# Kernel optimization log

Hardware: AMD Instinct MI355X
Metric: run time of the kernel (lower is better)

Reference implementation:

```python
import jax, jax.numpy as jnp
import numpy as np

# Config from module init / global Args
H = 8        # n_head
DK = 64      # d_k
DV = 64      # d_v
D = 512      # d_model
KSZ = 3      # kernel_size (args.kernel_size)
B_PARAM = 0.001
CUR_HEAD = 3
ALPHA_C = -float(np.log(B_PARAM / (H - 1) * CUR_HEAD))  # alpha_c (nonzero head)
EPS = 1e-6


def setup_inputs() -> dict:
    key = jax.random.key(0)
    ks = jax.random.split(key, 8)
    B, L = 2, 2048
    q = jax.random.normal(ks[0], (B, L, D), jnp.float32)
    k = jax.random.normal(ks[1], (B, L, D), jnp.float32)
    v = jax.random.normal(ks[2], (B, L, D), jnp.float32)
    # Linear weights stored torch-style: [out_features, in_features]
    w_q = jax.random.normal(ks[3], (H * DK, D), jnp.float32) * 0.02
    w_k = jax.random.normal(ks[4], (H * DK, D), jnp.float32) * 0.02
    w_v = jax.random.normal(ks[5], (H * DV, D), jnp.float32) * 0.02
    w_fc = jax.random.normal(ks[6], (D, H * DV), jnp.float32) * 0.02
    gamma = jnp.ones((D,), jnp.float32)
    beta = jnp.zeros((D,), jnp.float32)
    return {"q": q, "k": k, "v": v, "w_q": w_q, "w_k": w_k, "w_v": w_v,
            "w_fc": w_fc, "gamma": gamma, "beta": beta}


def reference(q, k, v, w_q, w_k, w_v, w_fc, gamma, beta):
    B, L, _ = q.shape
    residual = q
    # QKV projections -> [B, H, L, d]
    qh = jnp.einsum('bld,ed->ble', q, w_q).reshape(B, L, H, DK).transpose(0, 2, 1, 3)
    kh = jnp.einsum('bld,ed->ble', k, w_k).reshape(B, L, H, DK).transpose(0, 2, 1, 3)
    vh = jnp.einsum('bld,ed->ble', v, w_v).reshape(B, L, H, DV).transpose(0, 2, 1, 3)
    # Scores: matmul(q / sqrt(d_k), k^T)  (LaSAttention receives d_k = d_k**0.5)
    attn = jnp.einsum('bhqd,bhkd->bhqk', qh, kh) / jnp.sqrt(jnp.float32(DK))
    # Distance weighting: eld = alpha_c * -(x - y) * attn, d_l[i,j] = j - i
    idx = jnp.arange(L)
    d_l = idx[None, :] - idx[:, None]                      # [L, L]
    eld_mat = (-ALPHA_C * d_l).astype(attn.dtype)
    eld = eld_mat[None, None, :, :] * attn
    # Softmax then avg_pool1d(kernel=KSZ, stride=1, pad=(KSZ-1)//2, count_include_pad)
    p = jax.nn.softmax(eld, axis=-1)                       # [B, H, L, L]
    pad = (KSZ - 1) // 2
    pp = jnp.pad(p, ((0, 0), (0, 0), (0, 0), (pad, pad)))
    pooled = sum(pp[..., j:j + L] for j in range(KSZ)) / jnp.float32(KSZ)
    # Value matmul (seq lengths equal so no trimming needed)
    out = jnp.einsum('bhqk,bhkd->bhqd', pooled, vh)
    out = out.transpose(0, 2, 1, 3).reshape(B, L, H * DV)
    # Output projection (dropout is identity in eval), residual, LayerNorm
    out = jnp.einsum('ble,de->bld', out, w_fc)
    out = out[:, :, None, :] + residual[:, :, None, :]     # [B, L, 1, D]
    mu = out.mean(axis=-1, keepdims=True)
    var = ((out - mu) ** 2).mean(axis=-1, keepdims=True)
    out = (out - mu) / jnp.sqrt(var + EPS) * gamma + beta
    return (out, pooled)
```

## Files before the change

### kernel.cpp

```cpp
#include <hip/hip_runtime.h>
#include <cstddef>
#include <cstdint>

#define ALPHA_C 7.7550531393693407f
constexpr int BB = 2;
constexpr int LL = 2048;
constexpr int HH = 8;
constexpr size_t OUT0  = (size_t)BB * LL * 512;
constexpr size_t PLANE = (size_t)BB * HH * LL * 64;
constexpr size_t XN    = (size_t)BB * LL * 512;
constexpr size_t WN    = (size_t)512 * 512;

typedef __attribute__((ext_vector_type(8))) short bf16x8;
typedef __attribute__((ext_vector_type(4))) short short4v;
typedef __attribute__((ext_vector_type(4))) float f32x4;

__device__ inline short f2bf(float x) {
  union { float f; unsigned u; } un; un.f = x;
  unsigned r = un.u + 0x7fffu + ((un.u >> 16) & 1u);
  return (short)(r >> 16);
}
__device__ inline float bf2f(short s) {
  union { unsigned u; float f; } un; un.u = ((unsigned)(unsigned short)s) << 16;
  return un.f;
}
__device__ inline void split3(float x, short& h, short& m, short& l) {
  h = f2bf(x); float r = x - bf2f(h);
  m = f2bf(r); float r2 = r - bf2f(m);
  l = f2bf(r2);
}

__global__ __launch_bounds__(256) void k_split3x(
    const float* __restrict__ a, const float* __restrict__ b, const float* __restrict__ c,
    short* __restrict__ da, short* __restrict__ db, short* __restrict__ dc, size_t n)
{
  size_t i = ((size_t)blockIdx.x * 256 + threadIdx.x) * 4;
  if (i >= n) return;
  const float* srcs[3] = {a, b, c};
  short* dsts[3] = {da, db, dc};
  #pragma unroll
  for (int s = 0; s < 3; ++s) {
    float4 x = *(const float4*)&srcs[s][i];
    short4v h, m, l;
    short th, tm, tl;
    split3(x.x, th, tm, tl); h[0] = th; m[0] = tm; l[0] = tl;
    split3(x.y, th, tm, tl); h[1] = th; m[1] = tm; l[1] = tl;
    split3(x.z, th, tm, tl); h[2] = th; m[2] = tm; l[2] = tl;
    split3(x.w, th, tm, tl); h[3] = th; m[3] = tm; l[3] = tl;
    *(short4v*)&dsts[s][i]         = h;
    *(short4v*)&dsts[s][n + i]     = m;
    *(short4v*)&dsts[s][2 * n + i] = l;
  }
}

__global__ __launch_bounds__(256) void k_cvtbf(
    const float* __restrict__ src, short* __restrict__ dst, size_t n)
{
  size_t i = ((size_t)blockIdx.x * 256 + threadIdx.x) * 8;
  if (i >= n) return;
  float4 a = *(const float4*)&src[i];
  float4 b = *(const float4*)&src[i + 4];
  bf16x8 o;
  o[0] = f2bf(a.x); o[1] = f2bf(a.y); o[2] = f2bf(a.z); o[3] = f2bf(a.w);
  o[4] = f2bf(b.x); o[5] = f2bf(b.y); o[6] = f2bf(b.z); o[7] = f2bf(b.w);
  *(bf16x8*)&dst[i] = o;
}

__global__ __launch_bounds__(256) void k_vavg(
    const short* __restrict__ vt, short* __restrict__ vavgt)
{
  const size_t row = blockIdx.x;
  const short* src = vt + row * LL;
  short* dst = vavgt + row * LL;
  const int c0 = threadIdx.x * 8;
  bf16x8 x = *(const bf16x8*)&src[c0];
  float xf[10];
  xf[0] = (c0 > 0) ? bf2f(src[c0 - 1]) : 0.f;
  #pragma unroll
  for (int i = 0; i < 8; ++i) xf[i + 1] = bf2f(x[i]);
  xf[9] = (c0 + 8 < LL) ? bf2f(src[c0 + 8]) : 0.f;
  bf16x8 o;
  #pragma unroll
  for (int i = 0; i < 8; ++i) o[i] = f2bf((xf[i] + xf[i + 1] + xf[i + 2]) * (1.0f / 3.0f));
  *(bf16x8*)&dst[c0] = o;
}

__global__ __launch_bounds__(256) void k_proj(
    const short* __restrict__ xq, const short* __restrict__ xk, const short* __restrict__ xv,
    const short* __restrict__ wq3, const short* __restrict__ wk3, const short* __restrict__ wv3,
    short* __restrict__ qs, short* __restrict__ ks, short* __restrict__ vt)
{
  const int bx  = blockIdx.x;
  const int sel = bx >> 3;
  const int n0  = (bx & 7) * 64;
  const int m0  = blockIdx.y * 64;
  const short* X = sel == 0 ? xq  : (sel == 1 ? xk  : xv);
  const short* W = sel == 0 ? wq3 : (sel == 1 ? wk3 : wv3);

  __shared__ short Xs[3][64 * 72];
  __shared__ short Ws[3][64 * 72];
  const int tid = threadIdx.x;
  const int lane = tid & 63, w = tid >> 6;
  const int quad = lane >> 4, l15 = lane & 15, colg = l15;
  const int sr8 = tid >> 3, sc8 = (tid & 7) * 8;

  f32x4 acc[4];
  #pragma unroll
  for (int t = 0; t < 4; ++t) { acc[t][0]=0.f; acc[t][1]=0.f; acc[t][2]=0.f; acc[t][3]=0.f; }

  for (int kt = 0; kt < 8; ++kt) {
    const int k0 = kt * 64;
    #pragma unroll
    for (int p = 0; p < 3; ++p) {
      #pragma unroll
      for (int it = 0; it < 2; ++it) {
        int r = it * 32 + sr8;
        *(bf16x8*)&Xs[p][r * 72 + sc8] = *(const bf16x8*)&X[p * XN + (size_t)(m0 + r) * 512 + k0 + sc8];
        *(bf16x8*)&Ws[p][r * 72 + sc8] = *(const bf16x8*)&W[p * WN + (size_t)(n0 + r) * 512 + k0 + sc8];
      }
    }
    __syncthreads();
    #pragma unroll
    for (int ch = 0; ch < 2; ++ch) {
      const int ka = (quad << 3) + ch * 32;
      const int ar = (w * 16 + l15) * 72 + ka;
      bf16x8 ah = *(const bf16x8*)&Xs[0][ar];
      bf16x8 am = *(const bf16x8*)&Xs[1][ar];
      bf16x8 al = *(const bf16x8*)&Xs[2][ar];
      #pragma unroll
      for (int t = 0; t < 4; ++t) {
        const int br = (t * 16 + l15) * 72 + ka;
        bf16x8 bh_ = *(const bf16x8*)&Ws[0][br];
        bf16x8 bm_ = *(const bf16x8*)&Ws[1][br];
        bf16x8 bl_ = *(const bf16x8*)&Ws[2][br];
        acc[t] = __builtin_amdgcn_mfma_f32_16x16x32_bf16(ah, bh_, acc[t], 0, 0, 0);
        acc[t] = __builtin_amdgcn_mfma_f32_16x16x32_bf16(ah, bm_, acc[t], 0, 0, 0);
        acc[t] = __builtin_amdgcn_mfma_f32_16x16x32_bf16(am, bh_, acc[t], 0, 0, 0);
        acc[t] = __builtin_amdgcn_mfma_f32_16x16x32_bf16(ah, bl_, acc[t], 0, 0, 0);
        acc[t] = __builtin_amdgcn_mfma_f32_16x16x32_bf16(al, bh_, acc[t], 0, 0, 0);
        acc[t] = __builtin_amdgcn_mfma_f32_16x16x32_bf16(am, bm_, acc[t], 0, 0, 0);
      }
    }
    __syncthreads();
  }

  if (sel < 2) {
    short* Y = sel == 0 ? qs : ks;
    #pragma unroll
    for (int t = 0; t < 4; ++t) {
      const int e = n0 + t * 16 + colg, h = e >> 6, dk = e & 63;
      #pragma unroll
      for (int r = 0; r < 4; ++r) {
        const int m = m0 + w * 16 + quad * 4 + r;
        const int b = m >> 11, l = m & 2047;
        size_t base = ((size_t)(b * HH + h) * LL + l) * 64 + dk;
        short hh, mm, ll; split3(acc[t][r], hh, mm, ll);
        Y[base] = hh; Y[PLANE + base] = mm; Y[2 * PLANE + base] = ll;
      }
    }
  } else {
    const int b  = m0 >> 11;
    const int l0 = (m0 & 2047) + w * 16 + quad * 4;
    #pragma unroll
    for (int t = 0; t < 4; ++t) {
      const int e = n0 + t * 16 + colg, h = e >> 6, dk = e & 63;
      short4v s;
      #pragma unroll
      for (int r = 0; r < 4; ++r) s[r] = f2bf(acc[t][r]);
      *(short4v*)&vt[(((size_t)b * HH + h) * 64 + dk) * LL + l0] = s;
    }
  }
}

__global__ __launch_bounds__(256) void k_stats(
    const short* __restrict__ qs, const short* __restrict__ ks,
    float* __restrict__ statspart)
{
  const int i0 = blockIdx.x * 64;
  const int jh = blockIdx.y;
  const int bh = blockIdx.z;
  __shared__ short Ks[3][64 * 72];
  const int tid = threadIdx.x;
  const int lane = tid & 63, w = tid >> 6;
  const int quad = lane >> 4, colg = lane & 15, l15 = lane & 15;
  const int sr8 = tid >> 3, sc8 = (tid & 7) * 8;

  bf16x8 qf[3][2];
  {
    const size_t qoff = ((size_t)bh * LL + i0 + w * 16 + l15) * 64 + (quad << 3);
    #pragma unroll
    for (int p = 0; p < 3; ++p)
      #pragma unroll
      for (int ch = 0; ch < 2; ++ch)
        qf[p][ch] = *(const bf16x8*)&qs[p * PLANE + qoff + ch * 32];
  }

  const int jt0 = jh * 16;
  const short* kbase = ks + (size_t)bh * LL * 64;
  #pragma unroll
  for (int p = 0; p < 3; ++p)
    #pragma unroll
    for (int it = 0; it < 2; ++it) {
      int r = it * 32 + sr8;
      *(bf16x8*)&Ks[p][r * 72 + sc8] =
          *(const bf16x8*)&kbase[p * PLANE + ((size_t)jt0 * 64 + r) * 64 + sc8];
    }
  __syncthreads();

  float M[4], S[4];
  #pragma unroll
  for (int r = 0; r < 4; ++r) { M[r] = -3.0e38f; S[r] = 0.f; }

  for (int jj = 0; jj < 16; ++jj) {
    const int jt = jt0 + jj;
    const int j0 = jt * 64;
    bf16x8 kreg[3][2];
    if (jj + 1 < 16) {
      #pragma unroll
      for (int p = 0; p < 3; ++p)
        #pragma unroll
        for (int it = 0; it < 2; ++it) {
          int r = it * 32 + sr8;
          kreg[p][it] = *(const bf16x8*)&kbase[p * PLANE + ((size_t)(jt + 1) * 64 + r) * 64 + sc8];
        }
    }

    f32x4 acc[4];
    #pragma unroll
    for (int t = 0; t < 4; ++t) { acc[t][0]=0.f; acc[t][1]=0.f; acc[t][2]=0.f; acc[t][3]=0.f; }
    #pragma unroll
    for (int ch = 0; ch < 2; ++ch) {
      const int ka = (quad << 3) + ch * 32;
      #pragma unroll
      for (int t = 0; t < 4; ++t) {
        const int br = (t * 16 + l15) * 72 + ka;
        bf16x8 bh_ = *(const bf16x8*)&Ks[0][br];
        bf16x8 bm_ = *(const bf16x8*)&Ks[1][br];
        bf16x8 bl_ = *(const bf16x8*)&Ks[2][br];
        acc[t] = __builtin_amdgcn_mfma_f32_16x16x32_bf16(qf[0][ch], bh_, acc[t], 0, 0, 0);
        acc[t] = __builtin_amdgcn_mfma_f32_16x16x32_bf16(qf[0][ch], bm_, acc[t], 0, 0, 0);
        acc[t] = __builtin_amdgcn_mfma_f32_16x16x32_bf16(qf[1][ch], bh_, acc[t], 0, 0, 0);
        acc[t] = __builtin_amdgcn_mfma_f32_16x16x32_bf16(qf[0][ch], bl_, acc[t], 0, 0, 0);
        acc[t] = __builtin_amdgcn_mfma_f32_16x16x32_bf16(qf[2][ch], bh_, acc[t], 0, 0, 0);
        acc[t] = __builtin_amdgcn_mfma_f32_16x16x32_bf16(qf[1][ch], bm_, acc[t], 0, 0, 0);
      }
    }

    #pragma unroll
    for (int r = 0; r < 4; ++r) {
      const int irow = i0 + w * 16 + quad * 4 + r;
      float e0 = -ALPHA_C * (float)(j0 +  0 + colg - irow) * (acc[0][r] * 0.125f);
      float e1 = -ALPHA_C * (float)(j0 + 16 + colg - irow) * (acc[1][r] * 0.125f);
      float e2 = -ALPHA_C * (float)(j0 + 32 + colg - irow) * (acc[2][r] * 0.125f);
      float e3 = -ALPHA_C * (float)(j0 + 48 + colg - irow) * (acc[3][r] * 0.125f);
      float mx = fmaxf(fmaxf(e0, e1), fmaxf(e2, e3));
      float nM = fmaxf(M[r], mx);
      S[r] = S[r] * __expf(M[r] - nM)
           + __expf(e0 - nM) + __expf(e1 - nM) + __expf(e2 - nM) + __expf(e3 - nM);
      M[r] = nM;
    }

    __syncthreads();
    if (jj + 1 < 16) {
      #pragma unroll
      for (int p = 0; p < 3; ++p)
        #pragma unroll
        for (int it = 0; it < 2; ++it) {
          int r = it * 32 + sr8;
          *(bf16x8*)&Ks[p][r * 72 + sc8] = kreg[p][it];
        }
    }
    __syncthreads();
  }

  #pragma unroll
  for (int r = 0; r < 4; ++r) {
    float M_ = M[r], S_ = S[r];
    #pragma unroll
    for (int d = 1; d < 16; d <<= 1) {
      float Mo = __shfl_xor(M_, d);
      float So = __shfl_xor(S_, d);
      float nM = fmaxf(M_, Mo);
      S_ = S_ * __expf(M_ - nM) + So * __expf(Mo - nM);
      M_ = nM;
    }
    if (colg == 0) {
      int irow = i0 + w * 16 + quad * 4 + r;
      size_t idx = (((size_t)jh * 16 + bh) * LL + irow) * 2;
      statspart[idx] = M_; statspart[idx + 1] = S_;
    }
  }
}

__global__ __launch_bounds__(256) void k_mergestats(
    const float* __restrict__ statspart, float* __restrict__ rowstats)
{
  const size_t row = (size_t)blockIdx.x * 256 + threadIdx.x;
  float2 a = *(const float2*)&statspart[row * 2];
  float2 b = *(const float2*)&statspart[(size_t)16 * LL * 2 + row * 2];
  float nM = fmaxf(a.x, b.x);
  float S = a.y * __expf(a.x - nM) + b.y * __expf(b.x - nM);
  rowstats[row * 2] = nM; rowstats[row * 2 + 1] = S;
}

__global__ __launch_bounds__(256) void k_pool_pv(
    const short* __restrict__ qs, const short* __restrict__ ks,
    const short* __restrict__ vavgt, const float* __restrict__ rowstats,
    float* __restrict__ pooled, short* __restrict__ outh)
{
  const int i0 = blockIdx.x * 64;
  const int bh = blockIdx.y;
  const int b = bh >> 3, h = bh & 7;
  float*       Pg = pooled + (size_t)bh * LL * LL;
  const short* Vt = vavgt + (size_t)bh * 64 * LL;
  const short* kbase = ks + (size_t)bh * LL * 64;

  __shared__ short Ks[3][64 * 72];
  __shared__ short Vsm[64 * 72];
  __shared__ short Pa[2][64 * 72];
  __shared__ float Mrow[64], invSr[64], lhalo[64];

  const int tid = threadIdx.x;
  const int lane = tid & 63, w = tid >> 6;
  const int quad = lane >> 4, colg = lane & 15, l15 = lane & 15;
  const int sr8 = tid >> 3, sc8 = (tid & 7) * 8;

  bf16x8 qf[3][2];
  {
    const size_t qoff = ((size_t)bh * LL + i0 + w * 16 + l15) * 64 + (quad << 3);
    #pragma unroll
    for (int p = 0; p < 3; ++p)
      #pragma unroll
      for (int ch = 0; ch < 2; ++ch)
        qf[p][ch] = *(const bf16x8*)&qs[p * PLANE + qoff + ch * 32];
  }
  if (tid < 64) {
    float2 ms = *(const float2*)&rowstats[((size_t)bh * LL + i0 + tid) * 2];
    Mrow[tid] = ms.x; invSr[tid] = 1.0f / ms.y; lhalo[tid] = 0.f;
  }

  #pragma unroll
  for (int p = 0; p < 3; ++p)
    #pragma unroll
    for (int it = 0; it < 2; ++it) {
      int r = it * 32 + sr8;
      *(bf16x8*)&Ks[p][r * 72 + sc8] = *(const bf16x8*)&kbase[p * PLANE + (size_t)r * 64 + sc8];
    }
  __syncthreads();

  f32x4 pv[4];
  #pragma unroll
  for (int t = 0; t < 4; ++t) { pv[t][0]=0.f; pv[t][1]=0.f; pv[t][2]=0.f; pv[t][3]=0.f; }

  for (int jt = 0; jt <= 32; ++jt) {
    if (jt < 32) {
      const int j0 = jt * 64;
      f32x4 acc[4];
      #pragma unroll
      for (int t = 0; t < 4; ++t) { acc[t][0]=0.f; acc[t][1]=0.f; acc[t][2]=0.f; acc[t][3]=0.f; }
      #pragma unroll
      for (int ch = 0; ch < 2; ++ch) {
        const int ka = (quad << 3) + ch * 32;
        #pragma unroll
        for (int t = 0; t < 4; ++t) {
          const int br = (t * 16 + l15) * 72 + ka;
          bf16x8 bh_ = *(const bf16x8*)&Ks[0][br];
          bf16x8 bm_ = *(const bf16x8*)&Ks[1][br];
          bf16x8 bl_ = *(const bf16x8*)&Ks[2][br];
          acc[t] = __builtin_amdgcn_mfma_f32_16x16x32_bf16(qf[0][ch], bh_, acc[t], 0, 0, 0);
          acc[t] = __builtin_amdgcn_mfma_f32_16x16x32_bf16(qf[0][ch], bm_, acc[t], 0, 0, 0);
          acc[t] = __builtin_amdgcn_mfma_f32_16x16x32_bf16(qf[1][ch], bh_, acc[t], 0, 0, 0);
          acc[t] = __builtin_amdgcn_mfma_f32_16x16x32_bf16(qf[0][ch], bl_, acc[t], 0, 0, 0);
          acc[t] = __builtin_amdgcn_mfma_f32_16x16x32_bf16(qf[2][ch], bh_, acc[t], 0, 0, 0);
          acc[t] = __builtin_amdgcn_mfma_f32_16x16x32_bf16(qf[1][ch], bm_, acc[t], 0, 0, 0);
        }
      }
      short* Pc = Pa[jt & 1];
      #pragma unroll
      for (int r = 0; r < 4; ++r) {
        const int row = w * 16 + quad * 4 + r;
        const int irow = i0 + row;
        const float Mr = Mrow[row], iS = invSr[row];
        #pragma unroll
        for (int t = 0; t < 4; ++t) {
          int jl = t * 16 + colg;
          float e = -ALPHA_C * (float)(j0 + jl - irow) * (acc[t][r] * 0.125f);
          Pc[row * 72 + jl] = f2bf(__expf(e - Mr) * iS);
        }
      }
    }
    if (jt >= 1) {
      #pragma unroll
      for (int it = 0; it < 2; ++it) {
        int d = it * 32 + sr8;
        *(bf16x8*)&Vsm[d * 72 + sc8] = *(const bf16x8*)&Vt[(size_t)d * LL + (jt - 1) * 64 + sc8];
      }
    }
    __syncthreads();

    if (jt >= 1) {
      const short* Pp = Pa[(jt - 1) & 1];
      const short* Pn = Pa[jt & 1];
      #pragma unroll
      for (int u = 0; u < 2; ++u) {
        const int row = (u == 0) ? (tid >> 3) : (tid >> 3) + 32;
        const int c0 = (tid & 7) * 8;
        bf16x8 x = *(const bf16x8*)&Pp[row * 72 + c0];
        float xf[8];
        #pragma unroll
        for (int i = 0; i < 8; ++i) xf[i] = bf2f(x[i]);
        float lft = (c0 == 0)  ? lhalo[row] : bf2f(Pp[row * 72 + c0 - 1]);
        float rgt = (c0 == 56) ? ((jt < 32) ? bf2f(Pn[row * 72]) : 0.f)
                               : bf2f(Pp[row * 72 + c0 + 8]);
        f32x4 o0, o1;
        o0[0] = (lft   + xf[0] + xf[1]) * (1.0f/3.0f);
        o0[1] = (xf[0] + xf[1] + xf[2]) * (1.0f/3.0f);
        o0[2] = (xf[1] + xf[2] + xf[3]) * (1.0f/3.0f);
        o0[3] = (xf[2] + xf[3] + xf[4]) * (1.0f/3.0f);
        o1[0] = (xf[3] + xf[4] + xf[5]) * (1.0f/3.0f);
        o1[1] = (xf[4] + xf[5] + xf[6]) * (1.0f/3.0f);
        o1[2] = (xf[5] + xf[6] + xf[7]) * (1.0f/3.0f);
        o1[3] = (xf[6] + xf[7] + rgt  ) * (1.0f/3.0f);
        float* dst = &Pg[(size_t)(i0 + row) * LL + (jt - 1) * 64 + c0];
        __builtin_nontemporal_store(o0, (f32x4*)dst);
        __builtin_nontemporal_store(o1, (f32x4*)(dst + 4));
        if (c0 == 56) lhalo[row] = xf[7];
      }
      #pragma unroll
      for (int ch = 0; ch < 2; ++ch) {
        const int ka = (quad << 3) + ch * 32;
        bf16x8 af = *(const bf16x8*)&Pp[(w * 16 + l15) * 72 + ka];
        #pragma unroll
        for (int t = 0; t < 4; ++t) {
          bf16x8 bfv = *(const bf16x8*)&Vsm[(t * 16 + l15) * 72 + ka];
          pv[t] = __builtin_amdgcn_mfma_f32_16x16x32_bf16(af, bfv, pv[t], 0, 0, 0);
        }
      }
    }
    if (jt + 1 < 32) {
      #pragma unroll
      for (int p = 0; p < 3; ++p)
        #pragma unroll
        for (int it = 0; it < 2; ++it) {
          int r = it * 32 + sr8;
          *(bf16x8*)&Ks[p][r * 72 + sc8] =
              *(const bf16x8*)&kbase[p * PLANE + ((size_t)(jt + 1) * 64 + r) * 64 + sc8];
        }
    }
    __syncthreads();
  }

  #pragma unroll
  for (int t = 0; t < 4; ++t)
    #pragma unroll
    for (int r = 0; r < 4; ++r) {
      int i = i0 + w * 16 + quad * 4 + r;
      int d = t * 16 + colg;
      outh[((size_t)b * LL + i) * 512 + h * 64 + d] = f2bf(pv[t][r]);
    }
}

__global__ __launch_bounds__(256) void k_fc(
    const short* __restrict__ outh, const short* __restrict__ wfcb, float* __restrict__ fcout)
{
  const int n0 = blockIdx.x * 64;
  const int m0 = blockIdx.y * 64;
  __shared__ short Asm[64 * 72];
  __shared__ short Bsm[64 * 72];
  const int tid = threadIdx.x;
  const int lane = tid & 63, w = tid >> 6;
  const int sr8 = tid >> 3, sc8 = (tid & 7) * 8;

  f32x4 acc[4];
  #pragma unroll
  for (int t = 0; t < 4; ++t) { acc[t][0]=0.f; acc[t][1]=0.f; acc[t][2]=0.f; acc[t][3]=0.f; }

  for (int k0 = 0; k0 < 512; k0 += 64) {
    #pragma unroll
    for (int it = 0; it < 2; ++it) {
      int r = it * 32 + sr8;
      *(bf16x8*)&Asm[r * 72 + sc8] = *(const bf16x8*)&outh[(size_t)(m0 + r) * 512 + k0 + sc8];
      *(bf16x8*)&Bsm[r * 72 + sc8] = *(const bf16x8*)&wfcb[(size_t)(n0 + r) * 512 + k0 + sc8];
    }
    __syncthreads();
    #pragma unroll
    for (int ch = 0; ch < 2; ++ch) {
      const int ka = ((lane >> 4) << 3) + ch * 32;
      bf16x8 af = *(const bf16x8*)&Asm[(w * 16 + (lane & 15)) * 72 + ka];
      #pragma unroll
      for (int t = 0; t < 4; ++t) {
        bf16x8 bfv = *(const bf16x8*)&Bsm[(t * 16 + (lane & 15)) * 72 + ka];
        acc[t] = __builtin_amdgcn_mfma_f32_16x16x32_bf16(af, bfv, acc[t], 0, 0, 0);
      }
    }
    __syncthreads();
  }
  const int q4 = lane >> 4, colg = lane & 15;
  #pragma unroll
  for (int t = 0; t < 4; ++t)
    #pragma unroll
    for (int r = 0; r < 4; ++r) {
      int m = m0 + w * 16 + q4 * 4 + r;
      fcout[(size_t)m * 512 + n0 + t * 16 + colg] = acc[t][r];
    }
}

__global__ __launch_bounds__(256) void k_ln(
    const float* __restrict__ fcout, const float* __restrict__ resid,
    const float* __restrict__ gamma, const float* __restrict__ beta,
    float* __restrict__ out)
{
  const size_t row = blockIdx.x;
  const int tid = threadIdx.x;
  __shared__ float red[256];

  float x0 = fcout[row * 512 + tid]       + resid[row * 512 + tid];
  float x1 = fcout[row * 512 + 256 + tid] + resid[row * 512 + 256 + tid];

  red[tid] = x0 + x1; __syncthreads();
  for (int off = 128; off > 0; off >>= 1) {
    if (tid < off) red[tid] += red[tid + off];
    __syncthreads();
  }
  const float mu = red[0] * (1.0f / 512.0f); __syncthreads();

  float d0 = x0 - mu, d1 = x1 - mu;
  red[tid] = d0 * d0 + d1 * d1; __syncthreads();
  for (int off = 128; off > 0; off >>= 1) {
    if (tid < off) red[tid] += red[tid + off];
    __syncthreads();
  }
  const float var = red[0] * (1.0f / 512.0f);
  const float rstd = 1.0f / sqrtf(var + 1e-6f);

  out[row * 512 + tid]       = d0 * rstd * gamma[tid]       + beta[tid];
  out[row * 512 + 256 + tid] = d1 * rstd * gamma[tid + 256] + beta[tid + 256];
}

extern "C" void kernel_launch(void* const* d_in, const int* in_sizes, int n_in,
                              void* d_out, int out_size, void* d_ws, size_t ws_size,
                              hipStream_t stream)
{
  const float* q     = (const float*)d_in[0];
  const float* k     = (const float*)d_in[1];
  const float* v     = (const float*)d_in[2];
  const float* wq    = (const float*)d_in[3];
  const float* wk    = (const float*)d_in[4];
  const float* wv    = (const float*)d_in[5];
  const float* wfc   = (const float*)d_in[6];
  const float* gamma = (const float*)d_in[7];
  const float* beta  = (const float*)d_in[8];

  float* out    = (float*)d_out;
  float* pooled = out + OUT0;

  short* xq    = (short*)d_ws;
  short* xk    = xq + 3 * XN;
  short* xv    = xk + 3 * XN;
  short* wq3   = xv + 3 * XN;
  short* wk3   = wq3 + 3 * WN;
  short* wv3   = wk3 + 3 * WN;
  short* qsp   = wv3 + 3 * WN;
  short* ksp   = qsp + 3 * PLANE;
  short* vt    = ksp + 3 * PLANE;
  short* vavgt = vt + PLANE;
  short* wfcb  = vavgt + PLANE;
  short* outh  = wfcb + WN;
  float* statspart = (float*)(outh + OUT0);
  float* rowstats  = statspart + 4 * (size_t)BB * HH * LL;
  float* fcout     = rowstats + 2 * (size_t)BB * HH * LL;

  k_split3x<<<dim3((unsigned)(XN / 4 / 256)), 256, 0, stream>>>(q, k, v, xq, xk, xv, XN);
  k_split3x<<<dim3((unsigned)(WN / 4 / 256)), 256, 0, stream>>>(wq, wk, wv, wq3, wk3, wv3, WN);
  k_cvtbf  <<<dim3((unsigned)(WN / 8 / 256)), 256, 0, stream>>>(wfc, wfcb, WN);
  k_proj   <<<dim3(24, 64), 256, 0, stream>>>(xq, xk, xv, wq3, wk3, wv3, qsp, ksp, vt);
  k_vavg   <<<dim3(1024),   256, 0, stream>>>(vt, vavgt);
  k_stats  <<<dim3(32, 2, 16), 256, 0, stream>>>(qsp, ksp, statspart);
  k_mergestats<<<dim3(128), 256, 0, stream>>>(statspart, rowstats);
  k_pool_pv<<<dim3(32, 16), 256, 0, stream>>>(qsp, ksp, vavgt, rowstats, pooled, outh);
  k_fc     <<<dim3(8, 64),  256, 0, stream>>>(outh, wfcb, fcout);
  k_ln     <<<dim3(4096),   256, 0, stream>>>(fcout, q, gamma, beta, out);
}
```

Baseline: 496.7 us.

## Cache unnormalized exp scores in bf16 to skip recomputing QK in pool pass

The stats kernel now writes per-tile unnormalized exponentials (bf16) and per-tile running maxima to a large workspace buffer. The pool/PV kernel reads these back and rescales them instead of recomputing the 6-pass split-bf16 QK^T MFMA product. It is also split into two j-halves with a partial-sum merge kernel for more parallelism. This trades heavy MFMA recompute for an extra 128MB write and read of bf16 scores, plus an extra launch, and reuses the input-split workspace region for the score buffer.

```diff
diff --git a/kernel.cpp b/kernel.cpp
--- a/kernel.cpp
+++ b/kernel.cpp
@@ -10,6 +10,7 @@
 constexpr size_t PLANE = (size_t)BB * HH * LL * 64;
 constexpr size_t XN    = (size_t)BB * LL * 512;
 constexpr size_t WN    = (size_t)512 * 512;
+constexpr size_t UGN   = (size_t)BB * HH * LL * LL;
 
 typedef __attribute__((ext_vector_type(8))) short bf16x8;
 typedef __attribute__((ext_vector_type(4))) short short4v;
@@ -172,14 +173,16 @@
   }
 }
 
-__global__ __launch_bounds__(256) void k_stats(
+__global__ __launch_bounds__(256) void k_stats_u(
     const short* __restrict__ qs, const short* __restrict__ ks,
-    float* __restrict__ statspart)
+    float* __restrict__ statspart, short* __restrict__ ug,
+    float* __restrict__ mtile)
 {
   const int i0 = blockIdx.x * 64;
   const int jh = blockIdx.y;
   const int bh = blockIdx.z;
   __shared__ short Ks[3][64 * 72];
+  __shared__ short Us[64 * 72];
   const int tid = threadIdx.x;
   const int lane = tid & 63, w = tid >> 6;
   const int quad = lane >> 4, colg = lane & 15, l15 = lane & 15;
@@ -246,21 +249,40 @@
       }
     }
 
+    float mrow[4];
     #pragma unroll
     for (int r = 0; r < 4; ++r) {
-      const int irow = i0 + w * 16 + quad * 4 + r;
+      const int row = w * 16 + quad * 4 + r;
+      const int irow = i0 + row;
       float e0 = -ALPHA_C * (float)(j0 +  0 + colg - irow) * (acc[0][r] * 0.125f);
       float e1 = -ALPHA_C * (float)(j0 + 16 + colg - irow) * (acc[1][r] * 0.125f);
       float e2 = -ALPHA_C * (float)(j0 + 32 + colg - irow) * (acc[2][r] * 0.125f);
       float e3 = -ALPHA_C * (float)(j0 + 48 + colg - irow) * (acc[3][r] * 0.125f);
       float mx = fmaxf(fmaxf(e0, e1), fmaxf(e2, e3));
+      #pragma unroll
+      for (int d = 1; d < 16; d <<= 1) mx = fmaxf(mx, __shfl_xor(mx, d));
       float nM = fmaxf(M[r], mx);
-      S[r] = S[r] * __expf(M[r] - nM)
-           + __expf(e0 - nM) + __expf(e1 - nM) + __expf(e2 - nM) + __expf(e3 - nM);
+      float u0 = __expf(e0 - nM), u1 = __expf(e1 - nM);
+      float u2 = __expf(e2 - nM), u3 = __expf(e3 - nM);
+      S[r] = S[r] * __expf(M[r] - nM) + ((u0 + u1) + (u2 + u3));
       M[r] = nM;
-    }
-
-    __syncthreads();
+      mrow[r] = nM;
+      Us[row * 72 +      colg] = f2bf(u0);
+      Us[row * 72 + 16 + colg] = f2bf(u1);
+      Us[row * 72 + 32 + colg] = f2bf(u2);
+      Us[row * 72 + 48 + colg] = f2bf(u3);
+    }
+    if (colg == 0) {
+      f32x4 mm; mm[0] = mrow[0]; mm[1] = mrow[1]; mm[2] = mrow[2]; mm[3] = mrow[3];
+      *(f32x4*)&mtile[((size_t)(bh * 32 + jt)) * LL + i0 + w * 16 + quad * 4] = mm;
+    }
+
+    __syncthreads();
+    #pragma unroll
+    for (int it = 0; it < 2; ++it) {
+      int r = it * 32 + sr8;
+      *(bf16x8*)&ug[((size_t)bh * LL + i0 + r) * LL + j0 + sc8] = *(const bf16x8*)&Us[r * 72 + sc8];
+    }
     if (jj + 1 < 16) {
       #pragma unroll
       for (int p = 0; p < 3; ++p)
@@ -303,149 +325,112 @@
   rowstats[row * 2] = nM; rowstats[row * 2 + 1] = S;
 }
 
-__global__ __launch_bounds__(256) void k_pool_pv(
-    const short* __restrict__ qs, const short* __restrict__ ks,
+__global__ __launch_bounds__(256) void k_pv_pool(
+    const short* __restrict__ ug, const float* __restrict__ mtile,
     const short* __restrict__ vavgt, const float* __restrict__ rowstats,
-    float* __restrict__ pooled, short* __restrict__ outh)
+    float* __restrict__ pooled, float* __restrict__ pvpart)
 {
   const int i0 = blockIdx.x * 64;
   const int bh = blockIdx.y;
-  const int b = bh >> 3, h = bh & 7;
+  const int jz = blockIdx.z;
   float*       Pg = pooled + (size_t)bh * LL * LL;
   const short* Vt = vavgt + (size_t)bh * 64 * LL;
-  const short* kbase = ks + (size_t)bh * LL * 64;
-
-  __shared__ short Ks[3][64 * 72];
+  const short* Ub = ug + (size_t)bh * LL * LL;
+
+  __shared__ float Pf[64 * 72];
+  __shared__ short Pb[64 * 72];
   __shared__ short Vsm[64 * 72];
-  __shared__ short Pa[2][64 * 72];
   __shared__ float Mrow[64], invSr[64], lhalo[64];
 
   const int tid = threadIdx.x;
   const int lane = tid & 63, w = tid >> 6;
   const int quad = lane >> 4, colg = lane & 15, l15 = lane & 15;
-  const int sr8 = tid >> 3, sc8 = (tid & 7) * 8;
-
-  bf16x8 qf[3][2];
-  {
-    const size_t qoff = ((size_t)bh * LL + i0 + w * 16 + l15) * 64 + (quad << 3);
-    #pragma unroll
-    for (int p = 0; p < 3; ++p)
-      #pragma unroll
-      for (int ch = 0; ch < 2; ++ch)
-        qf[p][ch] = *(const bf16x8*)&qs[p * PLANE + qoff + ch * 32];
-  }
+  const int r8 = tid >> 3, c8 = (tid & 7) * 8;
+
   if (tid < 64) {
     float2 ms = *(const float2*)&rowstats[((size_t)bh * LL + i0 + tid) * 2];
-    Mrow[tid] = ms.x; invSr[tid] = 1.0f / ms.y; lhalo[tid] = 0.f;
-  }
-
-  #pragma unroll
-  for (int p = 0; p < 3; ++p)
+    Mrow[tid] = ms.x; invSr[tid] = 1.0f / ms.y;
+    float lh = 0.f;
+    if (jz > 0) {
+      float mt = mtile[((size_t)(bh * 32 + jz * 16 - 1)) * LL + i0 + tid];
+      lh = bf2f(Ub[(size_t)(i0 + tid) * LL + jz * 16 * 64 - 1]) * __expf(mt - ms.x) * (1.0f / ms.y);
+    }
+    lhalo[tid] = lh;
+  }
+  __syncthreads();
+
+  f32x4 pv[4];
+  #pragma unroll
+  for (int t = 0; t < 4; ++t) { pv[t][0]=0.f; pv[t][1]=0.f; pv[t][2]=0.f; pv[t][3]=0.f; }
+
+  for (int jt = jz * 16; jt < jz * 16 + 16; ++jt) {
+    const int j0 = jt * 64;
+    #pragma unroll
+    for (int uu = 0; uu < 2; ++uu) {
+      const int row = r8 + uu * 32;
+      bf16x8 x = *(const bf16x8*)&Ub[(size_t)(i0 + row) * LL + j0 + c8];
+      float mt = mtile[((size_t)(bh * 32 + jt)) * LL + i0 + row];
+      float sc = __expf(mt - Mrow[row]) * invSr[row];
+      f32x4 p0, p1; bf16x8 pb;
+      #pragma unroll
+      for (int i = 0; i < 4; ++i) {
+        float v0 = bf2f(x[i]) * sc;
+        float v1 = bf2f(x[i + 4]) * sc;
+        p0[i] = v0; p1[i] = v1;
+        pb[i] = f2bf(v0); pb[i + 4] = f2bf(v1);
+      }
+      *(f32x4*)&Pf[row * 72 + c8]     = p0;
+      *(f32x4*)&Pf[row * 72 + c8 + 4] = p1;
+      *(bf16x8*)&Pb[row * 72 + c8]    = pb;
+    }
     #pragma unroll
     for (int it = 0; it < 2; ++it) {
-      int r = it * 32 + sr8;
-      *(bf16x8*)&Ks[p][r * 72 + sc8] = *(const bf16x8*)&kbase[p * PLANE + (size_t)r * 64 + sc8];
-    }
-  __syncthreads();
-
-  f32x4 pv[4];
-  #pragma unroll
-  for (int t = 0; t < 4; ++t) { pv[t][0]=0.f; pv[t][1]=0.f; pv[t][2]=0.f; pv[t][3]=0.f; }
-
-  for (int jt = 0; jt <= 32; ++jt) {
-    if (jt < 32) {
-      const int j0 = jt * 64;
-      f32x4 acc[4];
-      #pragma unroll
-      for (int t = 0; t < 4; ++t) { acc[t][0]=0.f; acc[t][1]=0.f; acc[t][2]=0.f; acc[t][3]=0.f; }
-      #pragma unroll
-      for (int ch = 0; ch < 2; ++ch) {
-        const int ka = (quad << 3) + ch * 32;
-        #pragma unroll
-        for (int t = 0; t < 4; ++t) {
-          const int br = (t * 16 + l15) * 72 + ka;
-          bf16x8 bh_ = *(const bf16x8*)&Ks[0][br];
-          bf16x8 bm_ = *(const bf16x8*)&Ks[1][br];
-          bf16x8 bl_ = *(const bf16x8*)&Ks[2][br];
-          acc[t] = __builtin_amdgcn_mfma_f32_16x16x32_bf16(qf[0][ch], bh_, acc[t], 0, 0, 0);
-          acc[t] = __builtin_amdgcn_mfma_f32_16x16x32_bf16(qf[0][ch], bm_, acc[t], 0, 0, 0);
-          acc[t] = __builtin_amdgcn_mfma_f32_16x16x32_bf16(qf[1][ch], bh_, acc[t], 0, 0, 0);
-          acc[t] = __builtin_amdgcn_mfma_f32_16x16x32_bf16(qf[0][ch], bl_, acc[t], 0, 0, 0);
-          acc[t] = __builtin_amdgcn_mfma_f32_16x16x32_bf16(qf[2][ch], bh_, acc[t], 0, 0, 0);
-          acc[t] = __builtin_amdgcn_mfma_f32_16x16x32_bf16(qf[1][ch], bm_, acc[t], 0, 0, 0);
-        }
-      }
-      short* Pc = Pa[jt & 1];
-      #pragma unroll
-      for (int r = 0; r < 4; ++r) {
-        const int row = w * 16 + quad * 4 + r;
-        const int irow = i0 + row;
-        const float Mr = Mrow[row], iS = invSr[row];
-        #pragma unroll
-        for (int t = 0; t < 4; ++t) {
-          int jl = t * 16 + colg;
-          float e = -ALPHA_C * (float)(j0 + jl - irow) * (acc[t][r] * 0.125f);
-          Pc[row * 72 + jl] = f2bf(__expf(e - Mr) * iS);
-        }
-      }
-    }
-    if (jt >= 1) {
-      #pragma unroll
-      for (int it = 0; it < 2; ++it) {
-        int d = it * 32 + sr8;
-        *(bf16x8*)&Vsm[d * 72 + sc8] = *(const bf16x8*)&Vt[(size_t)d * LL + (jt - 1) * 64 + sc8];
-      }
-    }
-    __syncthreads();
-
-    if (jt >= 1) {
-      const short* Pp = Pa[(jt - 1) & 1];
-      const short* Pn = Pa[jt & 1];
-      #pragma unroll
-      for (int u = 0; u < 2; ++u) {
-        const int row = (u == 0) ? (tid >> 3) : (tid >> 3) + 32;
-        const int c0 = (tid & 7) * 8;
-        bf16x8 x = *(const bf16x8*)&Pp[row * 72 + c0];
-        float xf[8];
-        #pragma unroll
-        for (int i = 0; i < 8; ++i) xf[i] = bf2f(x[i]);
-        float lft = (c0 == 0)  ? lhalo[row] : bf2f(Pp[row * 72 + c0 - 1]);
-        float rgt = (c0 == 56) ? ((jt < 32) ? bf2f(Pn[row * 72]) : 0.f)
-                               : bf2f(Pp[row * 72 + c0 + 8]);
-        f32x4 o0, o1;
-        o0[0] = (lft   + xf[0] + xf[1]) * (1.0f/3.0f);
-        o0[1] = (xf[0] + xf[1] + xf[2]) * (1.0f/3.0f);
-        o0[2] = (xf[1] + xf[2] + xf[3]) * (1.0f/3.0f);
-        o0[3] = (xf[2] + xf[3] + xf[4]) * (1.0f/3.0f);
-        o1[0] = (xf[3] + xf[4] + xf[5]) * (1.0f/3.0f);
-        o1[1] = (xf[4] + xf[5] + xf[6]) * (1.0f/3.0f);
-        o1[2] = (xf[5] + xf[6] + xf[7]) * (1.0f/3.0f);
-        o1[3] = (xf[6] + xf[7] + rgt  ) * (1.0f/3.0f);
-        float* dst = &Pg[(size_t)(i0 + row) * LL + (jt - 1) * 64 + c0];
-        __builtin_nontemporal_store(o0, (f32x4*)dst);
-        __builtin_nontemporal_store(o1, (f32x4*)(dst + 4));
-        if (c0 == 56) lhalo[row] = xf[7];
-      }
-      #pragma unroll
-      for (int ch = 0; ch < 2; ++ch) {
-        const int ka = (quad << 3) + ch * 32;
-        bf16x8 af = *(const bf16x8*)&Pp[(w * 16 + l15) * 72 + ka];
-        #pragma unroll
-        for (int t = 0; t < 4; ++t) {
-          bf16x8 bfv = *(const bf16x8*)&Vsm[(t * 16 + l15) * 72 + ka];
-          pv[t] = __builtin_amdgcn_mfma_f32_16x16x32_bf16(af, bfv, pv[t], 0, 0, 0);
-        }
-      }
-    }
-    if (jt + 1 < 32) {
-      #pragma unroll
-      for (int p = 0; p < 3; ++p)
-        #pragma unroll
-        for (int it = 0; it < 2; ++it) {
-          int r = it * 32 + sr8;
-          *(bf16x8*)&Ks[p][r * 72 + sc8] =
-              *(const bf16x8*)&kbase[p * PLANE + ((size_t)(jt + 1) * 64 + r) * 64 + sc8];
-        }
+      int d = it * 32 + r8;
+      *(bf16x8*)&Vsm[d * 72 + c8] = *(const bf16x8*)&Vt[(size_t)d * LL + j0 + c8];
+    }
+    __syncthreads();
+
+    #pragma unroll
+    for (int uu = 0; uu < 2; ++uu) {
+      const int row = r8 + uu * 32;
+      const int irow = i0 + row;
+      f32x4 a0 = *(const f32x4*)&Pf[row * 72 + c8];
+      f32x4 a1 = *(const f32x4*)&Pf[row * 72 + c8 + 4];
+      float xf[8];
+      xf[0]=a0[0]; xf[1]=a0[1]; xf[2]=a0[2]; xf[3]=a0[3];
+      xf[4]=a1[0]; xf[5]=a1[1]; xf[6]=a1[2]; xf[7]=a1[3];
+      float lft, rgt;
+      lft = (c8 == 0) ? lhalo[row] : Pf[row * 72 + c8 - 1];
+      if (c8 == 56) {
+        if (jt + 1 < 32) {
+          float mt2 = mtile[((size_t)(bh * 32 + jt + 1)) * LL + irow];
+          float sc2 = __expf(mt2 - Mrow[row]) * invSr[row];
+          rgt = bf2f(Ub[(size_t)irow * LL + j0 + 64]) * sc2;
+        } else rgt = 0.f;
+      } else rgt = Pf[row * 72 + c8 + 8];
+      f32x4 o0, o1;
+      o0[0] = (lft   + xf[0] + xf[1]) * (1.0f/3.0f);
+      o0[1] = (xf[0] + xf[1] + xf[2]) * (1.0f/3.0f);
+      o0[2] = (xf[1] + xf[2] + xf[3]) * (1.0f/3.0f);
+      o0[3] = (xf[2] + xf[3] + xf[4]) * (1.0f/3.0f);
+      o1[0] = (xf[3] + xf[4] + xf[5]) * (1.0f/3.0f);
+      o1[1] = (xf[4] + xf[5] + xf[6]) * (1.0f/3.0f);
+      o1[2] = (xf[5] + xf[6] + xf[7]) * (1.0f/3.0f);
+      o1[3] = (xf[6] + xf[7] + rgt  ) * (1.0f/3.0f);
+      float* dst = &Pg[(size_t)irow * LL + j0 + c8];
+      __builtin_nontemporal_store(o0, (f32x4*)dst);
+      __builtin_nontemporal_store(o1, (f32x4*)(dst + 4));
+      if (c8 == 56) lhalo[row] = xf[7];
+    }
+    #pragma unroll
+    for (int ch = 0; ch < 2; ++ch) {
+      const int ka = (quad << 3) + ch * 32;
+      bf16x8 af = *(const bf16x8*)&Pb[(w * 16 + l15) * 72 + ka];
+      #pragma unroll
+      for (int t = 0; t < 4; ++t) {
+        bf16x8 bfv = *(const bf16x8*)&Vsm[(t * 16 + l15) * 72 + ka];
+        pv[t] = __builtin_amdgcn_mfma_f32_16x16x32_bf16(af, bfv, pv[t], 0, 0, 0);
+      }
     }
     __syncthreads();
   }
@@ -456,8 +441,24 @@
     for (int r = 0; r < 4; ++r) {
       int i = i0 + w * 16 + quad * 4 + r;
       int d = t * 16 + colg;
-      outh[((size_t)b * LL + i) * 512 + h * 64 + d] = f2bf(pv[t][r]);
-    }
+      pvpart[(((size_t)(jz * 16 + bh)) * LL + i) * 64 + d] = pv[t][r];
+    }
+}
+
+__global__ __launch_bounds__(256) void k_pvmerge(
+    const float* __restrict__ pvpart, short* __restrict__ outh)
+{
+  const size_t idx = ((size_t)blockIdx.x * 256 + threadIdx.x) * 4;
+  f32x4 a = *(const f32x4*)&pvpart[idx];
+  f32x4 b = *(const f32x4*)&pvpart[(size_t)16 * LL * 64 + idx];
+  const int bh = (int)(idx >> 17);
+  const int rem = (int)(idx & 131071);
+  const int i = rem >> 6, d = rem & 63;
+  const int bb = bh >> 3, h = bh & 7;
+  short4v o;
+  #pragma unroll
+  for (int t = 0; t < 4; ++t) o[t] = f2bf(a[t] + b[t]);
+  *(short4v*)&outh[((size_t)bb * LL + i) * 512 + h * 64 + d] = o;
 }
 
 __global__ __launch_bounds__(256) void k_fc(
@@ -554,13 +555,15 @@
   float* out    = (float*)d_out;
   float* pooled = out + OUT0;
 
-  short* xq    = (short*)d_ws;
+  short* ws_s  = (short*)d_ws;
+  short* xq    = ws_s;
   short* xk    = xq + 3 * XN;
   short* xv    = xk + 3 * XN;
   short* wq3   = xv + 3 * XN;
   short* wk3   = wq3 + 3 * WN;
   short* wv3   = wk3 + 3 * WN;
-  short* qsp   = wv3 + 3 * WN;
+  short* ug    = ws_s;
+  short* qsp   = ug + UGN;
   short* ksp   = qsp + 3 * PLANE;
   short* vt    = ksp + 3 * PLANE;
   short* vavgt = vt + PLANE;
@@ -568,16 +571,19 @@
   short* outh  = wfcb + WN;
   float* statspart = (float*)(outh + OUT0);
   float* rowstats  = statspart + 4 * (size_t)BB * HH * LL;
-  float* fcout     = rowstats + 2 * (size_t)BB * HH * LL;
+  float* mtile     = rowstats + 2 * (size_t)BB * HH * LL;
+  float* pvpart    = mtile + (size_t)16 * 32 * LL;
+  float* fcout     = (float*)d_ws;
 
   k_split3x<<<dim3((unsigned)(XN / 4 / 256)), 256, 0, stream>>>(q, k, v, xq, xk, xv, XN);
   k_split3x<<<dim3((unsigned)(WN / 4 / 256)), 256, 0, stream>>>(wq, wk, wv, wq3, wk3, wv3, WN);
   k_cvtbf  <<<dim3((unsigned)(WN / 8 / 256)), 256, 0, stream>>>(wfc, wfcb, WN);
   k_proj   <<<dim3(24, 64), 256, 0, stream>>>(xq, xk, xv, wq3, wk3, wv3, qsp, ksp, vt);
   k_vavg   <<<dim3(1024),   256, 0, stream>>>(vt, vavgt);
-  k_stats  <<<dim3(32, 2, 16), 256, 0, stream>>>(qsp, ksp, statspart);
+  k_stats_u<<<dim3(32, 2, 16), 256, 0, stream>>>(qsp, ksp, statspart, ug, mtile);
   k_mergestats<<<dim3(128), 256, 0, stream>>>(statspart, rowstats);
-  k_pool_pv<<<dim3(32, 16), 256, 0, stream>>>(qsp, ksp, vavgt, rowstats, pooled, outh);
+  k_pv_pool<<<dim3(32, 16, 2), 256, 0, stream>>>(ug, mtile, vavgt, rowstats, pooled, pvpart);
+  k_pvmerge<<<dim3(2048),   256, 0, stream>>>(pvpart, outh);
   k_fc     <<<dim3(8, 64),  256, 0, stream>>>(outh, wfcb, fcout);
   k_ln     <<<dim3(4096),   256, 0, stream>>>(fcout, q, gamma, beta, out);
 }
```

Measured after the change: 552.0 us. +11.1%, slower.

## Keep K fragments in registers, give each wave a column slice across all rows

Applied to the files above, without the earlier changes.

In both the stats and pool/PV kernels, each wave now holds all 64 query rows' Q fragments in registers and owns a 16-column slice of K loaded straight from global into registers, replacing the shared-memory K tile and its two barriers per step. The online softmax uses a wave-wide check to skip rescaling when no lane raises the max, with a final cross-wave merge through shared memory. The pool kernel folds max and log-sum into a single subtracted constant. Q register use grows fourfold, which may lower occupancy.

```diff
diff --git a/kernel.cpp b/kernel.cpp
--- a/kernel.cpp
+++ b/kernel.cpp
@@ -179,116 +179,110 @@
   const int i0 = blockIdx.x * 64;
   const int jh = blockIdx.y;
   const int bh = blockIdx.z;
-  __shared__ short Ks[3][64 * 72];
   const int tid = threadIdx.x;
   const int lane = tid & 63, w = tid >> 6;
   const int quad = lane >> 4, colg = lane & 15, l15 = lane & 15;
-  const int sr8 = tid >> 3, sc8 = (tid & 7) * 8;
-
-  bf16x8 qf[3][2];
-  {
-    const size_t qoff = ((size_t)bh * LL + i0 + w * 16 + l15) * 64 + (quad << 3);
+
+  bf16x8 qf[4][3][2];
+  #pragma unroll
+  for (int rg = 0; rg < 4; ++rg) {
+    const size_t qoff = ((size_t)bh * LL + i0 + rg * 16 + l15) * 64 + (quad << 3);
     #pragma unroll
     for (int p = 0; p < 3; ++p)
       #pragma unroll
       for (int ch = 0; ch < 2; ++ch)
-        qf[p][ch] = *(const bf16x8*)&qs[p * PLANE + qoff + ch * 32];
-  }
-
+        qf[rg][p][ch] = *(const bf16x8*)&qs[p * PLANE + qoff + ch * 32];
+  }
+
+  const short* kptr = ks + (size_t)bh * LL * 64 + (size_t)(w * 16 + l15) * 64 + (quad << 3);
   const int jt0 = jh * 16;
-  const short* kbase = ks + (size_t)bh * LL * 64;
+
+  bf16x8 kf[3][2];
   #pragma unroll
   for (int p = 0; p < 3; ++p)
     #pragma unroll
-    for (int it = 0; it < 2; ++it) {
-      int r = it * 32 + sr8;
-      *(bf16x8*)&Ks[p][r * 72 + sc8] =
-          *(const bf16x8*)&kbase[p * PLANE + ((size_t)jt0 * 64 + r) * 64 + sc8];
-    }
-  __syncthreads();
-
-  float M[4], S[4];
-  #pragma unroll
-  for (int r = 0; r < 4; ++r) { M[r] = -3.0e38f; S[r] = 0.f; }
-
+    for (int ch = 0; ch < 2; ++ch)
+      kf[p][ch] = *(const bf16x8*)&kptr[(size_t)jt0 * 4096 + p * PLANE + ch * 32];
+
+  float M[4][4], S[4][4];
+  #pragma unroll
+  for (int rg = 0; rg < 4; ++rg)
+    #pragma unroll
+    for (int r = 0; r < 4; ++r) { M[rg][r] = -3.0e38f; S[rg][r] = 0.f; }
+
+  const int jcol = w * 16 + colg;
   for (int jj = 0; jj < 16; ++jj) {
     const int jt = jt0 + jj;
     const int j0 = jt * 64;
-    bf16x8 kreg[3][2];
+
+    f32x4 acc[4];
+    #pragma unroll
+    for (int rg = 0; rg < 4; ++rg) { acc[rg][0]=0.f; acc[rg][1]=0.f; acc[rg][2]=0.f; acc[rg][3]=0.f; }
+    #pragma unroll
+    for (int ch = 0; ch < 2; ++ch) {
+      bf16x8 bh_ = kf[0][ch], bm_ = kf[1][ch], bl_ = kf[2][ch];
+      #pragma unroll
+      for (int rg = 0; rg < 4; ++rg) {
+        acc[rg] = __builtin_amdgcn_mfma_f32_16x16x32_bf16(qf[rg][0][ch], bh_, acc[rg], 0, 0, 0);
+        acc[rg] = __builtin_amdgcn_mfma_f32_16x16x32_bf16(qf[rg][0][ch], bm_, acc[rg], 0, 0, 0);
+        acc[rg] = __builtin_amdgcn_mfma_f32_16x16x32_bf16(qf[rg][1][ch], bh_, acc[rg], 0, 0, 0);
+        acc[rg] = __builtin_amdgcn_mfma_f32_16x16x32_bf16(qf[rg][0][ch], bl_, acc[rg], 0, 0, 0);
+        acc[rg] = __builtin_amdgcn_mfma_f32_16x16x32_bf16(qf[rg][2][ch], bh_, acc[rg], 0, 0, 0);
+        acc[rg] = __builtin_amdgcn_mfma_f32_16x16x32_bf16(qf[rg][1][ch], bm_, acc[rg], 0, 0, 0);
+      }
+    }
     if (jj + 1 < 16) {
       #pragma unroll
       for (int p = 0; p < 3; ++p)
         #pragma unroll
-        for (int it = 0; it < 2; ++it) {
-          int r = it * 32 + sr8;
-          kreg[p][it] = *(const bf16x8*)&kbase[p * PLANE + ((size_t)(jt + 1) * 64 + r) * 64 + sc8];
+        for (int ch = 0; ch < 2; ++ch)
+          kf[p][ch] = *(const bf16x8*)&kptr[(size_t)(jt + 1) * 4096 + p * PLANE + ch * 32];
+    }
+
+    #pragma unroll
+    for (int rg = 0; rg < 4; ++rg)
+      #pragma unroll
+      for (int r = 0; r < 4; ++r) {
+        const int irow = i0 + rg * 16 + quad * 4 + r;
+        float e = -ALPHA_C * (float)(j0 + jcol - irow) * (acc[rg][r] * 0.125f);
+        if (!__any(e > M[rg][r])) {
+          S[rg][r] += __expf(e - M[rg][r]);
+        } else {
+          float nM = fmaxf(M[rg][r], e);
+          S[rg][r] = S[rg][r] * __expf(M[rg][r] - nM) + __expf(e - nM);
+          M[rg][r] = nM;
         }
-    }
-
-    f32x4 acc[4];
-    #pragma unroll
-    for (int t = 0; t < 4; ++t) { acc[t][0]=0.f; acc[t][1]=0.f; acc[t][2]=0.f; acc[t][3]=0.f; }
-    #pragma unroll
-    for (int ch = 0; ch < 2; ++ch) {
-      const int ka = (quad << 3) + ch * 32;
-      #pragma unroll
-      for (int t = 0; t < 4; ++t) {
-        const int br = (t * 16 + l15) * 72 + ka;
-        bf16x8 bh_ = *(const bf16x8*)&Ks[0][br];
-        bf16x8 bm_ = *(const bf16x8*)&Ks[1][br];
-        bf16x8 bl_ = *(const bf16x8*)&Ks[2][br];
-        acc[t] = __builtin_amdgcn_mfma_f32_16x16x32_bf16(qf[0][ch], bh_, acc[t], 0, 0, 0);
-        acc[t] = __builtin_amdgcn_mfma_f32_16x16x32_bf16(qf[0][ch], bm_, acc[t], 0, 0, 0);
-        acc[t] = __builtin_amdgcn_mfma_f32_16x16x32_bf16(qf[1][ch], bh_, acc[t], 0, 0, 0);
-        acc[t] = __builtin_amdgcn_mfma_f32_16x16x32_bf16(qf[0][ch], bl_, acc[t], 0, 0, 0);
-        acc[t] = __builtin_amdgcn_mfma_f32_16x16x32_bf16(qf[2][ch], bh_, acc[t], 0, 0, 0);
-        acc[t] = __builtin_amdgcn_mfma_f32_16x16x32_bf16(qf[1][ch], bm_, acc[t], 0, 0, 0);
-      }
-    }
-
+      }
+  }
+
+  __shared__ float2 MSsm[4][64];
+  #pragma unroll
+  for (int rg = 0; rg < 4; ++rg)
     #pragma unroll
     for (int r = 0; r < 4; ++r) {
-      const int irow = i0 + w * 16 + quad * 4 + r;
-      float e0 = -ALPHA_C * (float)(j0 +  0 + colg - irow) * (acc[0][r] * 0.125f);
-      float e1 = -ALPHA_C * (float)(j0 + 16 + colg - irow) * (acc[1][r] * 0.125f);
-      float e2 = -ALPHA_C * (float)(j0 + 32 + colg - irow) * (acc[2][r] * 0.125f);
-      float e3 = -ALPHA_C * (float)(j0 + 48 + colg - irow) * (acc[3][r] * 0.125f);
-      float mx = fmaxf(fmaxf(e0, e1), fmaxf(e2, e3));
-      float nM = fmaxf(M[r], mx);
-      S[r] = S[r] * __expf(M[r] - nM)
-           + __expf(e0 - nM) + __expf(e1 - nM) + __expf(e2 - nM) + __expf(e3 - nM);
-      M[r] = nM;
-    }
-
-    __syncthreads();
-    if (jj + 1 < 16) {
-      #pragma unroll
-      for (int p = 0; p < 3; ++p)
-        #pragma unroll
-        for (int it = 0; it < 2; ++it) {
-          int r = it * 32 + sr8;
-          *(bf16x8*)&Ks[p][r * 72 + sc8] = kreg[p][it];
-        }
-    }
-    __syncthreads();
-  }
-
-  #pragma unroll
-  for (int r = 0; r < 4; ++r) {
-    float M_ = M[r], S_ = S[r];
-    #pragma unroll
-    for (int d = 1; d < 16; d <<= 1) {
-      float Mo = __shfl_xor(M_, d);
-      float So = __shfl_xor(S_, d);
-      float nM = fmaxf(M_, Mo);
-      S_ = S_ * __expf(M_ - nM) + So * __expf(Mo - nM);
-      M_ = nM;
-    }
-    if (colg == 0) {
-      int irow = i0 + w * 16 + quad * 4 + r;
-      size_t idx = (((size_t)jh * 16 + bh) * LL + irow) * 2;
-      statspart[idx] = M_; statspart[idx + 1] = S_;
-    }
+      float M_ = M[rg][r], S_ = S[rg][r];
+      #pragma unroll
+      for (int d = 1; d < 16; d <<= 1) {
+        float Mo = __shfl_xor(M_, d);
+        float So = __shfl_xor(S_, d);
+        float nM = fmaxf(M_, Mo);
+        S_ = S_ * __expf(M_ - nM) + So * __expf(Mo - nM);
+        M_ = nM;
+      }
+      if (colg == 0) MSsm[w][rg * 16 + quad * 4 + r] = make_float2(M_, S_);
+    }
+  __syncthreads();
+  if (tid < 64) {
+    float Mm = -3.0e38f, Sm = 0.f;
+    #pragma unroll
+    for (int ww = 0; ww < 4; ++ww) {
+      float2 p = MSsm[ww][tid];
+      float nM = fmaxf(Mm, p.x);
+      Sm = Sm * __expf(Mm - nM) + p.y * __expf(p.x - nM);
+      Mm = nM;
+    }
+    size_t idx = (((size_t)jh * 16 + bh) * LL + i0 + tid) * 2;
+    statspart[idx] = Mm; statspart[idx + 1] = Sm;
   }
 }
 
@@ -313,81 +307,79 @@
   const int b = bh >> 3, h = bh & 7;
   float*       Pg = pooled + (size_t)bh * LL * LL;
   const short* Vt = vavgt + (size_t)bh * 64 * LL;
-  const short* kbase = ks + (size_t)bh * LL * 64;
-
-  __shared__ short Ks[3][64 * 72];
+
   __shared__ short Vsm[64 * 72];
   __shared__ short Pa[2][64 * 72];
-  __shared__ float Mrow[64], invSr[64], lhalo[64];
+  __shared__ float lhalo[64];
 
   const int tid = threadIdx.x;
   const int lane = tid & 63, w = tid >> 6;
   const int quad = lane >> 4, colg = lane & 15, l15 = lane & 15;
   const int sr8 = tid >> 3, sc8 = (tid & 7) * 8;
 
-  bf16x8 qf[3][2];
-  {
-    const size_t qoff = ((size_t)bh * LL + i0 + w * 16 + l15) * 64 + (quad << 3);
+  bf16x8 qf[4][3][2];
+  #pragma unroll
+  for (int rg = 0; rg < 4; ++rg) {
+    const size_t qoff = ((size_t)bh * LL + i0 + rg * 16 + l15) * 64 + (quad << 3);
     #pragma unroll
     for (int p = 0; p < 3; ++p)
       #pragma unroll
       for (int ch = 0; ch < 2; ++ch)
-        qf[p][ch] = *(const bf16x8*)&qs[p * PLANE + qoff + ch * 32];
-  }
-  if (tid < 64) {
-    float2 ms = *(const float2*)&rowstats[((size_t)bh * LL + i0 + tid) * 2];
-    Mrow[tid] = ms.x; invSr[tid] = 1.0f / ms.y; lhalo[tid] = 0.f;
-  }
-
+        qf[rg][p][ch] = *(const bf16x8*)&qs[p * PLANE + qoff + ch * 32];
+  }
+  float C[4][4];
+  #pragma unroll
+  for (int rg = 0; rg < 4; ++rg)
+    #pragma unroll
+    for (int r = 0; r < 4; ++r) {
+      const int irow = i0 + rg * 16 + quad * 4 + r;
+      float2 ms = *(const float2*)&rowstats[((size_t)bh * LL + irow) * 2];
+      C[rg][r] = ms.x + __logf(ms.y);
+    }
+  if (tid < 64) lhalo[tid] = 0.f;
+
+  const short* kptr = ks + (size_t)bh * LL * 64 + (size_t)(w * 16 + l15) * 64 + (quad << 3);
+  bf16x8 kf[3][2];
   #pragma unroll
   for (int p = 0; p < 3; ++p)
     #pragma unroll
-    for (int it = 0; it < 2; ++it) {
-      int r = it * 32 + sr8;
-      *(bf16x8*)&Ks[p][r * 72 + sc8] = *(const bf16x8*)&kbase[p * PLANE + (size_t)r * 64 + sc8];
-    }
-  __syncthreads();
+    for (int ch = 0; ch < 2; ++ch)
+      kf[p][ch] = *(const bf16x8*)&kptr[p * PLANE + ch * 32];
 
   f32x4 pv[4];
   #pragma unroll
   for (int t = 0; t < 4; ++t) { pv[t][0]=0.f; pv[t][1]=0.f; pv[t][2]=0.f; pv[t][3]=0.f; }
 
+  const int jcol = w * 16 + colg;
   for (int jt = 0; jt <= 32; ++jt) {
     if (jt < 32) {
       const int j0 = jt * 64;
       f32x4 acc[4];
       #pragma unroll
-      for (int t = 0; t < 4; ++t) { acc[t][0]=0.f; acc[t][1]=0.f; acc[t][2]=0.f; acc[t][3]=0.f; }
+      for (int rg = 0; rg < 4; ++rg) { acc[rg][0]=0.f; acc[rg][1]=0.f; acc[rg][2]=0.f; acc[rg][3]=0.f; }
       #pragma unroll
       for (int ch = 0; ch < 2; ++ch) {
-        const int ka = (quad << 3) + ch * 32;
+        bf16x8 bh_ = kf[0][ch], bm_ = kf[1][ch], bl_ = kf[2][ch];
         #pragma unroll
-        for (int t = 0; t < 4; ++t) {
-          const int br = (t * 16 + l15) * 72 + ka;
-          bf16x8 bh_ = *(const bf16x8*)&Ks[0][br];
-          bf16x8 bm_ = *(const bf16x8*)&Ks[1][br];
-          bf16x8 bl_ = *(const bf16x8*)&Ks[2][br];
-          acc[t] = __builtin_amdgcn_mfma_f32_16x16x32_bf16(qf[0][ch], bh_, acc[t], 0, 0, 0);
-          acc[t] = __builtin_amdgcn_mfma_f32_16x16x32_bf16(qf[0][ch], bm_, acc[t], 0, 0, 0);
-          acc[t] = __builtin_amdgcn_mfma_f32_16x16x32_bf16(qf[1][ch], bh_, acc[t], 0, 0, 0);
-          acc[t] = __builtin_amdgcn_mfma_f32_16x16x32_bf16(qf[0][ch], bl_, acc[t], 0, 0, 0);
-          acc[t] = __builtin_amdgcn_mfma_f32_16x16x32_bf16(qf[2][ch], bh_, acc[t], 0, 0, 0);
-          acc[t] = __builtin_amdgcn_mfma_f32_16x16x32_bf16(qf[1][ch], bm_, acc[t], 0, 0, 0);
+        for (int rg = 0; rg < 4; ++rg) {
+          acc[rg] = __builtin_amdgcn_mfma_f32_16x16x32_bf16(qf[rg][0][ch], bh_, acc[rg], 0, 0, 0);
+          acc[rg] = __builtin_amdgcn_mfma_f32_16x16x32_bf16(qf[rg][0][ch], bm_, acc[rg], 0, 0, 0);
+          acc[rg] = __builtin_amdgcn_mfma_f32_16x16x32_bf16(qf[rg][1][ch], bh_, acc[rg], 0, 0, 0);
+          acc[rg] = __builtin_amdgcn_mfma_f32_16x16x32_bf16(qf[rg][0][ch], bl_, acc[rg], 0, 0, 0);
+          acc[rg] = __builtin_amdgcn_mfma_f32_16x16x32_bf16(qf[rg][2][ch], bh_, acc[rg], 0, 0, 0);
+          acc[rg] = __builtin_amdgcn_mfma_f32_16x16x32_bf16(qf[rg][1][ch], bm_, acc[rg], 0, 0, 0);
         }
       }
       short* Pc = Pa[jt & 1];
       #pragma unroll
-      for (int r = 0; r < 4; ++r) {
-        const int row = w * 16 + quad * 4 + r;
-        const int irow = i0 + row;
-        const float Mr = Mrow[row], iS = invSr[row];
+      for (int rg = 0; rg < 4; ++rg)
         #pragma unroll
-        for (int t = 0; t < 4; ++t) {
-          int jl = t * 16 + colg;
-          float e = -ALPHA_C * (float)(j0 + jl - irow) * (acc[t][r] * 0.125f);
-          Pc[row * 72 + jl] = f2bf(__expf(e - Mr) * iS);
+        for (int r = 0; r < 4; ++r) {
+          const int row = rg * 16 + quad * 4 + r;
+          const int irow = i0 + row;
+          float e = -ALPHA_C * (float)(j0 + jcol - irow) * (acc[rg][r] * 0.125f);
+          Pc[row * 72 + jcol] = f2bf(__expf(e - C[rg][r]));
         }
-      }
     }
     if (jt >= 1) {
       #pragma unroll
@@ -398,6 +390,13 @@
     }
     __syncthreads();
 
+    if (jt + 1 < 32) {
+      #pragma unroll
+      for (int p = 0; p < 3; ++p)
+        #pragma unroll
+        for (int ch = 0; ch < 2; ++ch)
+          kf[p][ch] = *(const bf16x8*)&kptr[(size_t)(jt + 1) * 4096 + p * PLANE + ch * 32];
+    }
     if (jt >= 1) {
       const short* Pp = Pa[(jt - 1) & 1];
       const short* Pn = Pa[jt & 1];
@@ -429,23 +428,13 @@
       #pragma unroll
       for (int ch = 0; ch < 2; ++ch) {
         const int ka = (quad << 3) + ch * 32;
-        bf16x8 af = *(const bf16x8*)&Pp[(w * 16 + l15) * 72 + ka];
+        bf16x8 af = *(const bf16x8*)&Pa[(jt - 1) & 1][(w * 16 + l15) * 72 + ka];
         #pragma unroll
         for (int t = 0; t < 4; ++t) {
           bf16x8 bfv = *(const bf16x8*)&Vsm[(t * 16 + l15) * 72 + ka];
           pv[t] = __builtin_amdgcn_mfma_f32_16x16x32_bf16(af, bfv, pv[t], 0, 0, 0);
         }
       }
-    }
-    if (jt + 1 < 32) {
-      #pragma unroll
-      for (int p = 0; p < 3; ++p)
-        #pragma unroll
-        for (int it = 0; it < 2; ++it) {
-          int r = it * 32 + sr8;
-          *(bf16x8*)&Ks[p][r * 72 + sc8] =
-              *(const bf16x8*)&kbase[p * PLANE + ((size_t)(jt + 1) * 64 + r) * 64 + sc8];
-        }
     }
     __syncthreads();
   }
```

Measured after the change: 555.7 us. 11.9% more time.
